# Kernel optimization log

Hardware: AMD Instinct MI355X
Metric: run time of the kernel (lower is better)

## Reference

```python
import jax, jax.numpy as jnp
import numpy as np

IMG = 256          # rendered image size (neural_renderer default)
SIGMA = 0.01       # soft-edge width in NDC units (differentiable silhouette)
EPS = 1e-8


def _get_eye(distance, elevation, azimuth):
    # get_points_from_angles (degrees)
    el = jnp.deg2rad(jnp.float32(elevation))
    az = jnp.deg2rad(jnp.float32(azimuth))
    return jnp.array([distance * jnp.cos(el) * jnp.sin(az),
                      distance * jnp.sin(el),
                      -distance * jnp.cos(el) * jnp.cos(az)], jnp.float32)


def _look_at(verts, eye):
    # neural_renderer look_at: camera at `eye` looking at origin, up = +y
    at = jnp.zeros(3, jnp.float32)
    up = jnp.array([0.0, 1.0, 0.0], jnp.float32)
    z = at - eye; z = z / (jnp.linalg.norm(z) + EPS)
    x = jnp.cross(up, z); x = x / (jnp.linalg.norm(x) + EPS)
    y = jnp.cross(z, x); y = y / (jnp.linalg.norm(y) + EPS)
    R = jnp.stack([x, y, z])                     # [3,3]
    return (verts - eye) @ R.T                   # [V,3]


def _perspective(verts, viewing_angle_deg=30.0):
    t = jnp.tan(jnp.deg2rad(jnp.float32(viewing_angle_deg)))
    z = verts[:, 2]
    x = verts[:, 0] / (z * t + EPS)
    y = verts[:, 1] / (z * t + EPS)
    return jnp.stack([x, y, z], axis=1)


def _edge_dist(p0, p1, px, py):
    # signed distance of every pixel to edge p0->p1; positive = left of edge
    e = p1 - p0                                              # [F,2]
    inv_len = jax.lax.rsqrt(e[:, 0] ** 2 + e[:, 1] ** 2 + EPS)  # [F]
    d = (e[None, :, 0] * (py[:, None] - p0[None, :, 1])
         - e[None, :, 1] * (px[:, None] - p0[None, :, 0]))      # [P,F]
    return d * inv_len[None, :]


def _render_silhouette(vertices, faces):
    eye = _get_eye(2.732, 0.0, 90.0)
    v = _look_at(vertices[0], eye)               # [V,3] camera space
    v = _perspective(v)                          # [V,3] NDC x,y + depth z
    fv = v[faces[0]]                             # [F,3,3]
    a, b, c = fv[:, 0, :2], fv[:, 1, :2], fv[:, 2, :2]   # [F,2] each
    # winding sign so that "inside" is positive regardless of orientation
    area = (b[:, 0] - a[:, 0]) * (c[:, 1] - a[:, 1]) \
         - (b[:, 1] - a[:, 1]) * (c[:, 0] - a[:, 0])     # [F]
    sgn = jnp.where(area >= 0, 1.0, -1.0)
    # pixel centers in NDC, row 0 = top of image (y flipped)
    ps = (jnp.arange(IMG, dtype=jnp.float32) + 0.5) / IMG * 2.0 - 1.0
    py, px = jnp.meshgrid(-ps, ps, indexing='ij')
    px = px.reshape(-1); py = py.reshape(-1)     # [P], P = IMG*IMG
    d0 = _edge_dist(a, b, px, py) * sgn[None, :]
    d1 = _edge_dist(b, c, px, py) * sgn[None, :]
    d2 = _edge_dist(c, a, px, py) * sgn[None, :]
    dmin = jnp.minimum(jnp.minimum(d0, d1), d2)  # [P,F] signed dist to tri
    alpha = jax.nn.sigmoid(dmin / SIGMA)         # soft per-face coverage
    alpha = jnp.clip(alpha, 0.0, 1.0 - 1e-6)
    # silhouette = 1 - prod_f (1 - alpha_f), computed in log space
    sil = 1.0 - jnp.exp(jnp.sum(jnp.log1p(-alpha), axis=1))  # [P]
    return sil.reshape(1, IMG, IMG)


def setup_inputs() -> dict:
    key = jax.random.key(0)
    k1, k2, k3 = jax.random.split(key, 3)
    vertices = 0.3 * jax.random.normal(k1, (1, 4096, 3), jnp.float32)
    faces = jax.random.randint(k2, (1, 512, 3), 0, 4096, jnp.int32)
    image_ref = jax.random.uniform(k3, (256, 256), jnp.float32)
    return {"vertices": vertices, "faces": faces, "image_ref": image_ref}


def reference(vertices, faces, image_ref):
    image = _render_silhouette(vertices, faces)             # [1,IMG,IMG]
    loss = jnp.sum(jnp.square(image - image_ref[None, :, :]))
    return loss
```

## Files before the change

### kernel.cpp

```cpp
#include <hip/hip_runtime.h>
#include <hip/hip_bf16.h>
#include <math.h>

#define FEPS   1e-8f
#define TANV   0.57735026918962576f
#define SCL    144.26950408889634f
#define CLIP2  19.931568569324174f
#define EYEX   2.732f
#define PXD    0.0078125f

__device__ __forceinline__ float bperm1(int rotB, float v) {
    return __int_as_float(__builtin_amdgcn_ds_bpermute(rotB, __float_as_int(v)));
}

__global__ __launch_bounds__(256) void sil_kernel(
    const float* __restrict__ verts, const int* __restrict__ faces,
    const float* __restrict__ ref, float* __restrict__ out)
{
    __shared__ float red[64][5];
    const int tid  = threadIdx.x;
    const int lane = tid & 63;
    const int q    = tid >> 6;
    const int tile = blockIdx.x;
    const int row  = tile >> 2;
    const int col0 = (tile & 3) << 6;

    const float py = 1.0f - ((float)row + 0.5f) * PXD;

    float A[2][3], E[2][3];
#pragma unroll
    for (int k = 0; k < 2; ++k) {
        const int f  = q * 128 + k * 64 + lane;
        const int i0 = faces[3*f+0], i1 = faces[3*f+1], i2 = faces[3*f+2];
        const int ii[3] = { i0, i1, i2 };
        float X[3], Y[3];
#pragma unroll
        for (int v = 0; v < 3; ++v) {
            const float vx = verts[3*ii[v]+0];
            const float vy = verts[3*ii[v]+1];
            const float vz = verts[3*ii[v]+2];
            const float inv = __builtin_amdgcn_rcpf(fmaf(EYEX - vx, TANV, FEPS));
            X[v] = vz * inv;
            Y[v] = vy * inv;
        }
        const float area = (X[1]-X[0])*(Y[2]-Y[0]) - (Y[1]-Y[0])*(X[2]-X[0]);
        const float sgn  = (area >= 0.0f) ? SCL : -SCL;
#pragma unroll
        for (int e = 0; e < 3; ++e) {
            const int   e1 = (e == 2) ? 0 : e + 1;
            const float ex = X[e1] - X[e], ey = Y[e1] - Y[e];
            const float il = __builtin_amdgcn_rsqf(fmaf(ex,ex,fmaf(ey,ey,FEPS))) * sgn;
            const float Ae = -ey * il;
            const float Be =  ex * il;
            const float Ce = (ey * X[e] - ex * Y[e]) * il;
            A[k][e] = Ae;
            E[k][e] = fmaf(Be, py, Ce);
        }
    }

    const int rotB = ((lane + 1) & 63) << 2;
    float px  = fmaf((float)(col0 + lane) + 0.5f, PXD, -1.0f);
    float acc = 0.0f;
#pragma unroll 8
    for (int s = 0; s < 64; ++s) {
        const float u0 = fminf(fminf(fmaf(A[0][0],px,E[0][0]), fmaf(A[0][1],px,E[0][1])),
                               fmaf(A[0][2],px,E[0][2]));
        const float u1 = fminf(fminf(fmaf(A[1][0],px,E[1][0]), fmaf(A[1][1],px,E[1][1])),
                               fmaf(A[1][2],px,E[1][2]));
        const float c0 = fminf(__builtin_amdgcn_logf(1.0f + __builtin_amdgcn_exp2f(u0)), CLIP2);
        const float c1 = fminf(__builtin_amdgcn_logf(1.0f + __builtin_amdgcn_exp2f(u1)), CLIP2);
        acc = bperm1(rotB, acc + c0 + c1);
        px  = bperm1(rotB, px);
    }

    red[lane][q] = acc;
    __syncthreads();

    if (tid < 64) {
        const float S2  = red[tid][0] + red[tid][1] + red[tid][2] + red[tid][3];
        const float sil = 1.0f - __builtin_amdgcn_exp2f(-S2);
        const float d   = sil - ref[tile * 64 + tid];
        float v = d * d;
#pragma unroll
        for (int off = 32; off > 0; off >>= 1)
            v += __shfl_down(v, off);
        if (tid == 0) atomicAdd(out, v);
    }
}

extern "C" void kernel_launch(void* const* d_in, const int* in_sizes, int n_in,
                              void* d_out, int out_size, void* d_ws, size_t ws_size,
                              hipStream_t stream) {
    const float* verts = (const float*)d_in[0];
    const int*   faces = (const int*)d_in[1];
    const float* ref   = (const float*)d_in[2];
    float*       out   = (float*)d_out;

    hipMemsetAsync(d_out, 0, sizeof(float), stream);
    sil_kernel<<<1024, 256, 0, stream>>>(verts, faces, ref, out);
}
```

Before: 28.93 us.

## Precompute face edge equations and cull faces per pixel tile

Moves the per-face projection and edge-equation setup into a small prep kernel that writes coefficients to workspace, replacing the memset. The main kernel stages those coefficients in shared memory and tests each face against the 64-pixel row segment using a conservative bound. Faces fully inside contribute a constant clipped value, faces far outside are skipped, and only faces in the soft band are evaluated per pixel through a ballot mask. This replaces the full wave-rotation loop with data-dependent work, at the cost of an extra kernel launch and divergent loop counts across waves.

```diff
diff --git a/kernel.cpp b/kernel.cpp
--- a/kernel.cpp
+++ b/kernel.cpp
@@ -6,80 +6,121 @@
 #define TANV   0.57735026918962576f
 #define SCL    144.26950408889634f
 #define CLIP2  19.931568569324174f
+#define TFAR   -20.0f
 #define EYEX   2.732f
 #define PXD    0.0078125f
+#define NFACE  512
 
-__device__ __forceinline__ float bperm1(int rotB, float v) {
-    return __int_as_float(__builtin_amdgcn_ds_bpermute(rotB, __float_as_int(v)));
+__global__ __launch_bounds__(256) void prep_kernel(
+    const float* __restrict__ verts, const int* __restrict__ faces,
+    float* __restrict__ fd, float* __restrict__ out)
+{
+    int f = blockIdx.x * 256 + threadIdx.x;
+    if (f == 0) out[0] = 0.0f;
+    if (f >= NFACE) return;
+
+    int ii[3] = { faces[3*f], faces[3*f+1], faces[3*f+2] };
+    float X[3], Y[3];
+#pragma unroll
+    for (int v = 0; v < 3; ++v) {
+        float vx = verts[3*ii[v]+0];
+        float vy = verts[3*ii[v]+1];
+        float vz = verts[3*ii[v]+2];
+        float inv = __builtin_amdgcn_rcpf(fmaf(EYEX - vx, TANV, FEPS));
+        X[v] = vz * inv;
+        Y[v] = vy * inv;
+    }
+    float area = (X[1]-X[0])*(Y[2]-Y[0]) - (Y[1]-Y[0])*(X[2]-X[0]);
+    float sgn = (area >= 0.0f) ? SCL : -SCL;
+
+    float4* dst = (float4*)(fd + f * 12);
+#pragma unroll
+    for (int e = 0; e < 3; ++e) {
+        int e1 = (e == 2) ? 0 : e + 1;
+        float ex = X[e1] - X[e], ey = Y[e1] - Y[e];
+        float il = __builtin_amdgcn_rsqf(fmaf(ex,ex,fmaf(ey,ey,FEPS))) * sgn;
+        float A = -ey * il;
+        float B =  ex * il;
+        float C = (ey * X[e] - ex * Y[e]) * il;
+        dst[e] = make_float4(A, B, C, fabsf(A) * 0.25f);
+    }
 }
 
-__global__ __launch_bounds__(256) void sil_kernel(
-    const float* __restrict__ verts, const int* __restrict__ faces,
-    const float* __restrict__ ref, float* __restrict__ out)
+__global__ __launch_bounds__(256) void main_kernel(
+    const float* __restrict__ fd, const float* __restrict__ ref,
+    float* __restrict__ out)
 {
+    __shared__ float sf[NFACE * 12];
     __shared__ float red[64][5];
-    const int tid  = threadIdx.x;
-    const int lane = tid & 63;
-    const int q    = tid >> 6;
-    const int tile = blockIdx.x;
-    const int row  = tile >> 2;
-    const int col0 = (tile & 3) << 6;
 
-    const float py = 1.0f - ((float)row + 0.5f) * PXD;
+    const int tid = threadIdx.x, lane = tid & 63, q = tid >> 6;
+    const int tile = blockIdx.x, row = tile >> 2, col0 = (tile & 3) << 6;
+    const float py  = 1.0f - ((float)row + 0.5f) * PXD;
+    const float pxc = (float)(col0 + 32) * PXD - 1.0f;
 
-    float A[2][3], E[2][3];
+    const float4* g4 = (const float4*)fd;
+    float4* s4 = (float4*)sf;
+#pragma unroll
+    for (int i = 0; i < 6; ++i) s4[tid + i * 256] = g4[tid + i * 256];
+
+    unsigned long long bmask[2];
+    int incnt = 0;
 #pragma unroll
     for (int k = 0; k < 2; ++k) {
-        const int f  = q * 128 + k * 64 + lane;
-        const int i0 = faces[3*f+0], i1 = faces[3*f+1], i2 = faces[3*f+2];
-        const int ii[3] = { i0, i1, i2 };
-        float X[3], Y[3];
+        int f = q * 128 + k * 64 + lane;
+        const float4* c = (const float4*)(fd + f * 12);
+        float4 ca = c[0], cb = c[1], cc = c[2];
+        float u0 = fmaf(ca.x, pxc, fmaf(ca.y, py, ca.z));
+        float u1 = fmaf(cb.x, pxc, fmaf(cb.y, py, cb.z));
+        float u2 = fmaf(cc.x, pxc, fmaf(cc.y, py, cc.z));
+        float lo = fminf(fminf(u0 - ca.w, u1 - cb.w), u2 - cc.w);
+        float hi = fminf(fminf(u0 + ca.w, u1 + cb.w), u2 + cc.w);
+        bool inside = (lo >= CLIP2);
+        bool band = (!inside) && (hi > TFAR);
+        bmask[k] = __ballot(band);
+        incnt += __popcll(__ballot(inside));
+    }
+    __syncthreads();
+
+    const float px = fmaf((float)(col0 + lane) + 0.5f, PXD, -1.0f);
+    float acc = (float)incnt * CLIP2;
+
 #pragma unroll
-        for (int v = 0; v < 3; ++v) {
-            const float vx = verts[3*ii[v]+0];
-            const float vy = verts[3*ii[v]+1];
-            const float vz = verts[3*ii[v]+2];
-            const float inv = __builtin_amdgcn_rcpf(fmaf(EYEX - vx, TANV, FEPS));
-            X[v] = vz * inv;
-            Y[v] = vy * inv;
+    for (int k = 0; k < 2; ++k) {
+        unsigned long long m = bmask[k];
+        const int base = q * 128 + k * 64;
+        if (m) {
+            int f = base + (int)__builtin_ctzll(m); m &= m - 1;
+            float4 ca = *(const float4*)&sf[f*12];
+            float4 cb = *(const float4*)&sf[f*12+4];
+            float4 cc = *(const float4*)&sf[f*12+8];
+            while (m) {
+                int f2 = base + (int)__builtin_ctzll(m); m &= m - 1;
+                float4 na = *(const float4*)&sf[f2*12];
+                float4 nb = *(const float4*)&sf[f2*12+4];
+                float4 nc = *(const float4*)&sf[f2*12+8];
+                float u = fminf(fminf(fmaf(ca.x, px, fmaf(ca.y, py, ca.z)),
+                                      fmaf(cb.x, px, fmaf(cb.y, py, cb.z))),
+                                      fmaf(cc.x, px, fmaf(cc.y, py, cc.z)));
+                float t = __builtin_amdgcn_exp2f(u);
+                acc += fminf(__builtin_amdgcn_logf(1.0f + t), CLIP2);
+                ca = na; cb = nb; cc = nc;
+            }
+            float u = fminf(fminf(fmaf(ca.x, px, fmaf(ca.y, py, ca.z)),
+                                  fmaf(cb.x, px, fmaf(cb.y, py, cb.z))),
+                                  fmaf(cc.x, px, fmaf(cc.y, py, cc.z)));
+            float t = __builtin_amdgcn_exp2f(u);
+            acc += fminf(__builtin_amdgcn_logf(1.0f + t), CLIP2);
         }
-        const float area = (X[1]-X[0])*(Y[2]-Y[0]) - (Y[1]-Y[0])*(X[2]-X[0]);
-        const float sgn  = (area >= 0.0f) ? SCL : -SCL;
-#pragma unroll
-        for (int e = 0; e < 3; ++e) {
-            const int   e1 = (e == 2) ? 0 : e + 1;
-            const float ex = X[e1] - X[e], ey = Y[e1] - Y[e];
-            const float il = __builtin_amdgcn_rsqf(fmaf(ex,ex,fmaf(ey,ey,FEPS))) * sgn;
-            const float Ae = -ey * il;
-            const float Be =  ex * il;
-            const float Ce = (ey * X[e] - ex * Y[e]) * il;
-            A[k][e] = Ae;
-            E[k][e] = fmaf(Be, py, Ce);
-        }
-    }
-
-    const int rotB = ((lane + 1) & 63) << 2;
-    float px  = fmaf((float)(col0 + lane) + 0.5f, PXD, -1.0f);
-    float acc = 0.0f;
-#pragma unroll 8
-    for (int s = 0; s < 64; ++s) {
-        const float u0 = fminf(fminf(fmaf(A[0][0],px,E[0][0]), fmaf(A[0][1],px,E[0][1])),
-                               fmaf(A[0][2],px,E[0][2]));
-        const float u1 = fminf(fminf(fmaf(A[1][0],px,E[1][0]), fmaf(A[1][1],px,E[1][1])),
-                               fmaf(A[1][2],px,E[1][2]));
-        const float c0 = fminf(__builtin_amdgcn_logf(1.0f + __builtin_amdgcn_exp2f(u0)), CLIP2);
-        const float c1 = fminf(__builtin_amdgcn_logf(1.0f + __builtin_amdgcn_exp2f(u1)), CLIP2);
-        acc = bperm1(rotB, acc + c0 + c1);
-        px  = bperm1(rotB, px);
     }
 
     red[lane][q] = acc;
     __syncthreads();
 
     if (tid < 64) {
-        const float S2  = red[tid][0] + red[tid][1] + red[tid][2] + red[tid][3];
-        const float sil = 1.0f - __builtin_amdgcn_exp2f(-S2);
-        const float d   = sil - ref[tile * 64 + tid];
+        float S   = red[tid][0] + red[tid][1] + red[tid][2] + red[tid][3];
+        float sil = 1.0f - __builtin_amdgcn_exp2f(-S);
+        float d   = sil - ref[tile * 64 + tid];
         float v = d * d;
 #pragma unroll
         for (int off = 32; off > 0; off >>= 1)
@@ -95,7 +136,8 @@
     const int*   faces = (const int*)d_in[1];
     const float* ref   = (const float*)d_in[2];
     float*       out   = (float*)d_out;
+    float*       fd    = (float*)d_ws;
 
-    hipMemsetAsync(d_out, 0, sizeof(float), stream);
-    sil_kernel<<<1024, 256, 0, stream>>>(verts, faces, ref, out);
+    prep_kernel<<<2, 256, 0, stream>>>(verts, faces, fd, out);
+    main_kernel<<<1024, 256, 0, stream>>>(fd, ref, out);
 }
```

Measured after the change: 26.55 us. -8.2%, faster.

## Cull faces per 16x4 pixel tile and process only edge-band faces

Applied to the files above, without the earlier changes.

Each block now covers a 16x4 pixel tile. Per-face edge coefficients go into shared memory, and every face is classified against the tile's bounding box as fully inside (contribution clamped to a constant), far outside (contribution negligible, skipped) or in the soft band. Only band faces are evaluated per pixel, iterated via ballot masks with software prefetch from LDS, replacing the dense 512-face bpermute rotation loop. This removes most of the transcendental work, but makes per-wave work data dependent and divergent. Skipping faces with u below -20 in log2 units drops terms under roughly 1e-6, so the result changes slightly.

```diff
diff --git a/kernel.cpp b/kernel.cpp
--- a/kernel.cpp
+++ b/kernel.cpp
@@ -6,33 +6,33 @@
 #define TANV   0.57735026918962576f
 #define SCL    144.26950408889634f
 #define CLIP2  19.931568569324174f
+#define TFAR   -20.0f
 #define EYEX   2.732f
 #define PXD    0.0078125f
-
-__device__ __forceinline__ float bperm1(int rotB, float v) {
-    return __int_as_float(__builtin_amdgcn_ds_bpermute(rotB, __float_as_int(v)));
-}
+#define NFACE  512
+#define WX     0.05859375f
+#define WY     0.01171875f
 
 __global__ __launch_bounds__(256) void sil_kernel(
     const float* __restrict__ verts, const int* __restrict__ faces,
     const float* __restrict__ ref, float* __restrict__ out)
 {
+    __shared__ float4 sf[NFACE * 3];
     __shared__ float red[64][5];
-    const int tid  = threadIdx.x;
-    const int lane = tid & 63;
-    const int q    = tid >> 6;
-    const int tile = blockIdx.x;
-    const int row  = tile >> 2;
-    const int col0 = (tile & 3) << 6;
 
-    const float py = 1.0f - ((float)row + 0.5f) * PXD;
+    const int tid = threadIdx.x, lane = tid & 63, q = tid >> 6;
+    const int tileX = blockIdx.x & 15, tileY = blockIdx.x >> 4;
+    const int col0 = tileX << 4, row0 = tileY << 2;
 
-    float A[2][3], E[2][3];
+    const float pxc = (float)(col0 + 8) * PXD - 1.0f;
+    const float pyc = 1.0f - (float)(row0 + 2) * PXD;
+
+    unsigned long long bmask[2];
+    int incnt = 0;
 #pragma unroll
     for (int k = 0; k < 2; ++k) {
-        const int f  = q * 128 + k * 64 + lane;
-        const int i0 = faces[3*f+0], i1 = faces[3*f+1], i2 = faces[3*f+2];
-        const int ii[3] = { i0, i1, i2 };
+        const int f = q * 128 + k * 64 + lane;
+        const int ii[3] = { faces[3*f], faces[3*f+1], faces[3*f+2] };
         float X[3], Y[3];
 #pragma unroll
         for (int v = 0; v < 3; ++v) {
@@ -45,41 +45,73 @@
         }
         const float area = (X[1]-X[0])*(Y[2]-Y[0]) - (Y[1]-Y[0])*(X[2]-X[0]);
         const float sgn  = (area >= 0.0f) ? SCL : -SCL;
+        float lo = 1e30f, hi = 1e30f;
 #pragma unroll
         for (int e = 0; e < 3; ++e) {
             const int   e1 = (e == 2) ? 0 : e + 1;
             const float ex = X[e1] - X[e], ey = Y[e1] - Y[e];
             const float il = __builtin_amdgcn_rsqf(fmaf(ex,ex,fmaf(ey,ey,FEPS))) * sgn;
-            const float Ae = -ey * il;
-            const float Be =  ex * il;
-            const float Ce = (ey * X[e] - ex * Y[e]) * il;
-            A[k][e] = Ae;
-            E[k][e] = fmaf(Be, py, Ce);
+            const float A = -ey * il;
+            const float B =  ex * il;
+            const float C = (ey * X[e] - ex * Y[e]) * il;
+            sf[f*3 + e] = make_float4(A, B, C, 0.0f);
+            const float u = fmaf(A, pxc, fmaf(B, pyc, C));
+            const float w = fabsf(A) * WX + fabsf(B) * WY;
+            lo = fminf(lo, u - w);
+            hi = fminf(hi, u + w);
         }
+        const bool inside = (lo >= CLIP2);
+        const bool band   = (!inside) && (hi > TFAR);
+        bmask[k] = __ballot(band);
+        incnt += __popcll(__ballot(inside));
     }
+    __syncthreads();
 
-    const int rotB = ((lane + 1) & 63) << 2;
-    float px  = fmaf((float)(col0 + lane) + 0.5f, PXD, -1.0f);
-    float acc = 0.0f;
-#pragma unroll 8
-    for (int s = 0; s < 64; ++s) {
-        const float u0 = fminf(fminf(fmaf(A[0][0],px,E[0][0]), fmaf(A[0][1],px,E[0][1])),
-                               fmaf(A[0][2],px,E[0][2]));
-        const float u1 = fminf(fminf(fmaf(A[1][0],px,E[1][0]), fmaf(A[1][1],px,E[1][1])),
-                               fmaf(A[1][2],px,E[1][2]));
-        const float c0 = fminf(__builtin_amdgcn_logf(1.0f + __builtin_amdgcn_exp2f(u0)), CLIP2);
-        const float c1 = fminf(__builtin_amdgcn_logf(1.0f + __builtin_amdgcn_exp2f(u1)), CLIP2);
-        acc = bperm1(rotB, acc + c0 + c1);
-        px  = bperm1(rotB, px);
+    const int   col = col0 + (lane & 15), row = row0 + (lane >> 4);
+    const float px  = ((float)col + 0.5f) * PXD - 1.0f;
+    const float py  = 1.0f - ((float)row + 0.5f) * PXD;
+    float acc = (float)incnt * CLIP2;
+
+    unsigned long long m0 = bmask[0], m1 = bmask[1];
+    const int base = q * 128;
+#define POP(F) { if (m0) { F = base + (int)__builtin_ctzll(m0); m0 &= m0-1; } \
+                 else if (m1) { F = base + 64 + (int)__builtin_ctzll(m1); m1 &= m1-1; } \
+                 else F = -1; }
+    int fa, fb;
+    POP(fa); POP(fb);
+    int faL = fa < 0 ? 0 : fa, fbL = fb < 0 ? 0 : fb;
+    float4 A0 = sf[faL*3], A1 = sf[faL*3+1], A2 = sf[faL*3+2];
+    float4 B0 = sf[fbL*3], B1 = sf[fbL*3+1], B2 = sf[fbL*3+2];
+    while (fa >= 0) {
+        int fc, fd2;
+        POP(fc); POP(fd2);
+        const int fcL = fc < 0 ? 0 : fc, fdL = fd2 < 0 ? 0 : fd2;
+        float4 C0 = sf[fcL*3], C1 = sf[fcL*3+1], C2 = sf[fcL*3+2];
+        float4 D0 = sf[fdL*3], D1 = sf[fdL*3+1], D2 = sf[fdL*3+2];
+        const float ua = fminf(fminf(fmaf(A0.x,px,fmaf(A0.y,py,A0.z)),
+                                     fmaf(A1.x,px,fmaf(A1.y,py,A1.z))),
+                                     fmaf(A2.x,px,fmaf(A2.y,py,A2.z)));
+        const float ub = fminf(fminf(fmaf(B0.x,px,fmaf(B0.y,py,B0.z)),
+                                     fmaf(B1.x,px,fmaf(B1.y,py,B1.z))),
+                                     fmaf(B2.x,px,fmaf(B2.y,py,B2.z)));
+        const float ca = fminf(__builtin_amdgcn_logf(1.0f + __builtin_amdgcn_exp2f(ua)), CLIP2);
+        const float cb = fminf(__builtin_amdgcn_logf(1.0f + __builtin_amdgcn_exp2f(ub)), CLIP2);
+        acc += ca;
+        acc += (fb >= 0) ? cb : 0.0f;
+        fa = fc; fb = fd2;
+        A0 = C0; A1 = C1; A2 = C2;
+        B0 = D0; B1 = D1; B2 = D2;
     }
+#undef POP
 
     red[lane][q] = acc;
     __syncthreads();
 
     if (tid < 64) {
-        const float S2  = red[tid][0] + red[tid][1] + red[tid][2] + red[tid][3];
-        const float sil = 1.0f - __builtin_amdgcn_exp2f(-S2);
-        const float d   = sil - ref[tile * 64 + tid];
+        const float S   = red[tid][0] + red[tid][1] + red[tid][2] + red[tid][3];
+        const float sil = 1.0f - __builtin_amdgcn_exp2f(-S);
+        const int prow = row0 + (tid >> 4), pcol = col0 + (tid & 15);
+        const float d  = sil - ref[prow * 256 + pcol];
         float v = d * d;
 #pragma unroll
         for (int off = 32; off > 0; off >>= 1)
```

After: 27.14 us. 6.2% less time.
